# Kernel tuning notes

Measured on AMD Instinct MI355X. Metric: run time of the kernel, lower is better.

The kernel has to match this reference:

```python
import jax, jax.numpy as jnp
import numpy as np

SCALE = 64.0  # quantization scale (step = 1/SCALE), also threshold clamp floor


def setup_inputs() -> dict:
    key = jax.random.key(0)
    x = jax.random.normal(key, (32, 2048, 512), dtype=jnp.float32)  # [B, C, T]
    threshold = jnp.array([0.1], dtype=jnp.float32)  # shared learnable threshold
    return {"x": x, "threshold": threshold}


def _delta_scan(x, thr):
    """Delta differential encoding with residual carry (cum_error=False).

    delta[t] = x[t] - x[t-1] + r[t-1]
    y[t]     = delta[t] if |delta[t]| >= thr else 0
    r[t]     = delta[t] - y[t]
    """
    xt = jnp.moveaxis(x, -1, 0)  # [T, B, C]
    zeros = jnp.zeros_like(xt[0])
    def step(carry, xi):
        pre, res = carry
        delta = xi - pre + res
        y = jnp.where(jnp.abs(delta) >= thr, delta, jnp.zeros_like(delta))
        return (xi, delta - y), y
    _, ys = jax.lax.scan(step, (zeros, zeros), xt)
    return jnp.moveaxis(ys, 0, -1)  # [B, C, T]


def reference(x, threshold):
    # threshold clamp to [1/scale, inf)
    thr = jnp.maximum(threshold, 1.0 / SCALE)
    y = _delta_scan(x, thr)
    # quantize(output, step=1/scale, mode=FLOOR)
    return jnp.floor(y * SCALE) / SCALE
```

## Files before the change

### kernel.cpp

```cpp
#include <hip/hip_runtime.h>


#define T_LEN 512

constexpr int BLOCK   = 256;
constexpr int ROWS_PB = 256;
constexpr int CF      = 64;
constexpr int CV      = CF / 4;
constexpr int NCHUNK  = T_LEN / CF;
constexpr int NROUND  = ROWS_PB * CV / BLOCK;

__global__ __launch_bounds__(BLOCK) void delta_scan_kernel(
    const float* __restrict__ x,
    const float* __restrict__ thrp,
    float* __restrict__ out)
{
    __shared__ float4 lds[ROWS_PB * CV];

    const int tid  = threadIdx.x;
    const int row0 = blockIdx.x * ROWS_PB;

    const float thr = fmaxf(thrp[0], 0.015625f);

    const float4* __restrict__ xv = reinterpret_cast<const float4*>(x);
    float4* __restrict__       ov = reinterpret_cast<float4*>(out);

    const size_t rbase = (size_t)(row0 + tid) * (T_LEN / 4);

    float pre = 0.0f, res = 0.0f;

#pragma unroll
    for (int c = 0; c < NCHUNK; ++c) {
        float4 v[CV];
#pragma unroll
        for (int i = 0; i < CV; ++i) v[i] = xv[rbase + c * CV + i];

#pragma unroll
        for (int i = 0; i < CV; ++i) {
            float4 q;
            { float d=(v[i].x-pre)+res; bool b=fabsf(d)>=thr; float y=b?d:0.0f;
              res=b?0.0f:d; pre=v[i].x; q.x=floorf(y*64.0f)*0.015625f; }
            { float d=(v[i].y-pre)+res; bool b=fabsf(d)>=thr; float y=b?d:0.0f;
              res=b?0.0f:d; pre=v[i].y; q.y=floorf(y*64.0f)*0.015625f; }
            { float d=(v[i].z-pre)+res; bool b=fabsf(d)>=thr; float y=b?d:0.0f;
              res=b?0.0f:d; pre=v[i].z; q.z=floorf(y*64.0f)*0.015625f; }
            { float d=(v[i].w-pre)+res; bool b=fabsf(d)>=thr; float y=b?d:0.0f;
              res=b?0.0f:d; pre=v[i].w; q.w=floorf(y*64.0f)*0.015625f; }

            lds[tid * CV + (i ^ (tid & 7))] = q;
        }
        __syncthreads();

#pragma unroll
        for (int k = 0; k < NROUND; ++k) {
            const int rr = k * (BLOCK / CV) + (tid >> 4);
            const int jj = tid & (CV - 1);
            const float4 t4 = lds[rr * CV + (jj ^ (rr & 7))];
            ov[(size_t)(row0 + rr) * (T_LEN / 4) + c * CV + jj] = t4;
        }
        __syncthreads();
    }
}

extern "C" void kernel_launch(void* const* d_in, const int* in_sizes, int n_in,
                              void* d_out, int out_size, void* d_ws, size_t ws_size,
                              hipStream_t stream)
{
    const float* x    = (const float*)d_in[0];
    const float* thrp = (const float*)d_in[1];
    float*       out  = (float*)d_out;

    const int rows = in_sizes[0] / T_LEN;
    const int grid = rows / ROWS_PB;

    delta_scan_kernel<<<grid, BLOCK, 0, stream>>>(x, thrp, out);
}
```

Measured before the change: 243.1 us.

## Double-buffer input chunks in registers and use per-wave LDS transpose without block barriers

Prefetches the next 64-element time chunk into a second register buffer while the current chunk is scanned, so global-load latency overlaps with the serial scan arithmetic. The LDS staging for coalesced stores is split into per-wave regions, so each wave transposes only its own 64 rows and the two __syncthreads per chunk are removed. The cost is doubled register use for the input buffers, with launch_bounds set to one block per SM to allow it, which may lower occupancy. Dropping the barriers relies on the LDS region being wave-private and the wave executing in lockstep.

Measured after the change: 240.5 us. No clear change (-1.1%).

```diff
diff --git a/kernel.cpp b/kernel.cpp
--- a/kernel.cpp
+++ b/kernel.cpp
@@ -4,61 +4,70 @@
 #define T_LEN 512
 
 constexpr int BLOCK   = 256;
-constexpr int ROWS_PB = 256;
-constexpr int CF      = 64;
-constexpr int CV      = CF / 4;
-constexpr int NCHUNK  = T_LEN / CF;
-constexpr int NROUND  = ROWS_PB * CV / BLOCK;
+constexpr int WAVE    = 64;
+constexpr int CV      = 16;
+constexpr int NCHUNK  = T_LEN / (CV * 4);
 
-__global__ __launch_bounds__(BLOCK) void delta_scan_kernel(
+__global__ __launch_bounds__(BLOCK, 1) void delta_scan_kernel(
     const float* __restrict__ x,
     const float* __restrict__ thrp,
     float* __restrict__ out)
 {
-    __shared__ float4 lds[ROWS_PB * CV];
+    __shared__ float4 lds[BLOCK / WAVE][WAVE * CV];
 
     const int tid  = threadIdx.x;
-    const int row0 = blockIdx.x * ROWS_PB;
+    const int wid  = tid >> 6;
+    const int lane = tid & 63;
+    float4* __restrict__ wlds = lds[wid];
+
+    const int row   = blockIdx.x * BLOCK + tid;
+    const int wrow0 = blockIdx.x * BLOCK + wid * WAVE;
 
     const float thr = fmaxf(thrp[0], 0.015625f);
 
     const float4* __restrict__ xv = reinterpret_cast<const float4*>(x);
     float4* __restrict__       ov = reinterpret_cast<float4*>(out);
-
-    const size_t rbase = (size_t)(row0 + tid) * (T_LEN / 4);
+    const size_t rbase = (size_t)row * (T_LEN / 4);
 
     float pre = 0.0f, res = 0.0f;
+    float4 va[CV], vb[CV];
+
+#pragma unroll
+    for (int i = 0; i < CV; ++i) va[i] = xv[rbase + i];
 
 #pragma unroll
     for (int c = 0; c < NCHUNK; ++c) {
-        float4 v[CV];
+        float4* cur = (c & 1) ? vb : va;
+        float4* nxt = (c & 1) ? va : vb;
+
+        if (c + 1 < NCHUNK) {
 #pragma unroll
-        for (int i = 0; i < CV; ++i) v[i] = xv[rbase + c * CV + i];
+            for (int i = 0; i < CV; ++i) nxt[i] = xv[rbase + (c + 1) * CV + i];
+        }
 
 #pragma unroll
         for (int i = 0; i < CV; ++i) {
+            float4 v = cur[i];
             float4 q;
-            { float d=(v[i].x-pre)+res; bool b=fabsf(d)>=thr; float y=b?d:0.0f;
-              res=b?0.0f:d; pre=v[i].x; q.x=floorf(y*64.0f)*0.015625f; }
-            { float d=(v[i].y-pre)+res; bool b=fabsf(d)>=thr; float y=b?d:0.0f;
-              res=b?0.0f:d; pre=v[i].y; q.y=floorf(y*64.0f)*0.015625f; }
-            { float d=(v[i].z-pre)+res; bool b=fabsf(d)>=thr; float y=b?d:0.0f;
-              res=b?0.0f:d; pre=v[i].z; q.z=floorf(y*64.0f)*0.015625f; }
-            { float d=(v[i].w-pre)+res; bool b=fabsf(d)>=thr; float y=b?d:0.0f;
-              res=b?0.0f:d; pre=v[i].w; q.w=floorf(y*64.0f)*0.015625f; }
+            { float d=(v.x-pre)+res; bool b=fabsf(d)>=thr; float y=b?d:0.0f;
+              res=b?0.0f:d; pre=v.x; q.x=floorf(y*64.0f)*0.015625f; }
+            { float d=(v.y-pre)+res; bool b=fabsf(d)>=thr; float y=b?d:0.0f;
+              res=b?0.0f:d; pre=v.y; q.y=floorf(y*64.0f)*0.015625f; }
+            { float d=(v.z-pre)+res; bool b=fabsf(d)>=thr; float y=b?d:0.0f;
+              res=b?0.0f:d; pre=v.z; q.z=floorf(y*64.0f)*0.015625f; }
+            { float d=(v.w-pre)+res; bool b=fabsf(d)>=thr; float y=b?d:0.0f;
+              res=b?0.0f:d; pre=v.w; q.w=floorf(y*64.0f)*0.015625f; }
 
-            lds[tid * CV + (i ^ (tid & 7))] = q;
+            wlds[lane * CV + (i ^ (lane & 7))] = q;
         }
-        __syncthreads();
 
 #pragma unroll
-        for (int k = 0; k < NROUND; ++k) {
-            const int rr = k * (BLOCK / CV) + (tid >> 4);
-            const int jj = tid & (CV - 1);
-            const float4 t4 = lds[rr * CV + (jj ^ (rr & 7))];
-            ov[(size_t)(row0 + rr) * (T_LEN / 4) + c * CV + jj] = t4;
+        for (int k = 0; k < 16; ++k) {
+            const int rr = k * 4 + (lane >> 4);
+            const int jj = lane & 15;
+            const float4 t4 = wlds[rr * CV + (jj ^ (rr & 7))];
+            ov[(size_t)(wrow0 + rr) * (T_LEN / 4) + c * CV + jj] = t4;
         }
-        __syncthreads();
     }
 }
 
@@ -71,7 +80,7 @@
     float*       out  = (float*)d_out;
 
     const int rows = in_sizes[0] / T_LEN;
-    const int grid = rows / ROWS_PB;
+    const int grid = rows / BLOCK;
 
     delta_scan_kernel<<<grid, BLOCK, 0, stream>>>(x, thrp, out);
 }
```
